# Performance work log

Hardware: AMD Instinct MI355X
Metric: run time of the kernel (lower is better)

The kernel has to match this reference:

```python
import jax, jax.numpy as jnp
import numpy as np

D = 2048        # input_size / model dim
H = 2816        # hidden_size per expert (GLU -> w1 has 2*H rows)
E = 8           # num_experts
M = 4096        # tokens (batch*seq)


def setup_inputs() -> dict:
    key = jax.random.key(0)
    k1, k2, k3, k4, k5 = jax.random.split(key, 5)
    x = jax.random.normal(k1, (M, D), dtype=jnp.float32)
    # ParallelExperts init: uniform(-1/fan_in_dim, 1/fan_in_dim); scale kept simple here
    w1 = jax.random.uniform(k2, (E, 2 * H, D), dtype=jnp.float32, minval=-1.0, maxval=1.0) / (2 * H)
    w2 = jax.random.uniform(k3, (E, D, H), dtype=jnp.float32, minval=-1.0, maxval=1.0) / D
    router_w = jax.random.normal(k4, (E, D), dtype=jnp.float32) * (1.0 / np.sqrt(D))
    bias = jnp.zeros((D,), dtype=jnp.float32)
    return {"x": x, "w1": w1, "w2": w2, "router_w": router_w, "bias": bias, "top_k": 2}


def _moe_forward(x, w1, w2, router_w, bias, top_k):
    # Router: logits -> softmax (fp32) -> top-k -> renormalize (fused_moe semantics)
    logits = x @ router_w.T                                # [M, E]
    probs = jax.nn.softmax(logits.astype(jnp.float32), axis=-1)
    topk_w, topk_ids = jax.lax.top_k(probs, top_k)         # [M, k]
    topk_w = topk_w / jnp.sum(topk_w, axis=-1, keepdims=True)
    # Dense combine weights [M, E]: gate weight if expert selected, else 0
    m = x.shape[0]
    combine = jnp.zeros((m, w1.shape[0]), dtype=x.dtype)
    combine = combine.at[jnp.arange(m)[:, None], topk_ids].add(topk_w.astype(x.dtype))
    # Grouped expert GEMMs, expressed as a loop over the small fixed expert set.
    # Contribution of expert e is masked by combine[:, e] (zero for unrouted tokens).
    y = jnp.zeros_like(x)
    hdim = w2.shape[2]
    for e in range(w1.shape[0]):
        g = x @ w1[e].T                                    # [M, 2H]
        h = jax.nn.silu(g[:, :hdim]) * g[:, hdim:]          # silu_and_mul (GLU)
        y = y + combine[:, e:e + 1] * (h @ w2[e].T)         # [M, D]
    return y + bias


def reference(x, w1, w2, router_w, bias, top_k):
    return _moe_forward(x, w1, w2, router_w, bias, top_k)
```

## Files before the change

### kernel.cpp

```cpp
#include <hip/hip_runtime.h>
#include <hip/hip_bf16.h>
#include <stdint.h>

#define M_TOK 4096
#define DDIM  2048
#define HDIM  2816
#define NEXP  8
#define PMAX  10240
#define MAXTILES 40
#define NB1   22
#define NB2   8
#define NT1   64
#define NT2   88

typedef __attribute__((ext_vector_type(8))) short short8;
typedef __attribute__((ext_vector_type(4))) float f32x4;

#define GLD16(g, l) __builtin_amdgcn_global_load_lds(                              \
    (const __attribute__((address_space(1))) unsigned int*)(g),                    \
    (__attribute__((address_space(3))) unsigned int*)(l), 16, 0, 0)

#define VMCNT(n) asm volatile("s_waitcnt vmcnt(" #n ")" ::: "memory")

__device__ __forceinline__ unsigned short f2bf(float f) {
  unsigned int u = __float_as_uint(f);
  u += 0x7fffu + ((u >> 16) & 1u);
  return (unsigned short)(u >> 16);
}
__device__ __forceinline__ float bf2f(unsigned short u) {
  return __uint_as_float(((unsigned)u) << 16);
}

#define GP0(KT, VM, STG)                                                         \
  { VMCNT(VM);                                                                   \
    __builtin_amdgcn_s_barrier();                                                \
    asm volatile("" ::: "memory");                                               \
    { const char* ab_ = ldsp + ((KT) & 3) * 16384;                               \
      const char* bb_ = ldsp + 65536 + ((KT) & 3) * 16384;                       \
      _Pragma("unroll") for (int mi = 0; mi < 4; ++mi)                           \
        av[mi] = *(const short8*)(ab_ + aoff[mi]);                               \
      _Pragma("unroll") for (int ni = 0; ni < 4; ++ni)                           \
        bv[ni] = *(const short8*)(bb_ + boff[ni]);                               \
      if (STG) { size_t kb_ = (size_t)((KT) + 3) * 64;                           \
        char* d_ = ldsp + (((KT) + 3) & 3) * 16384;                              \
        GLD16(aS0 + kb_, d_ + aD0); GLD16(aS1 + kb_, d_ + aD1); }                \
    }                                                                            \
    asm volatile("" ::: "memory");                                               \
    __builtin_amdgcn_s_barrier();                                                \
    __builtin_amdgcn_s_setprio(1);                                               \
    _Pragma("unroll") for (int mi = 0; mi < 4; ++mi)                             \
      _Pragma("unroll") for (int ni = 0; ni < 4; ++ni)                           \
        acc[mi][ni] = __builtin_amdgcn_mfma_f32_16x16x32_bf16(av[mi], bv[ni], acc[mi][ni], 0, 0, 0); \
    __builtin_amdgcn_s_setprio(0); }

#define GP1(KT, STG)                                                             \
  { __builtin_amdgcn_s_barrier();                                                \
    asm volatile("" ::: "memory");                                               \
    { const char* ab_ = ldsp + ((KT) & 3) * 16384;                               \
      _Pragma("unroll") for (int mi = 0; mi < 4; ++mi)                           \
        av[mi] = *(const short8*)(ab_ + aoff[4 + mi]);                           \
      if (STG) { size_t kb_ = (size_t)((KT) + 3) * 64;                           \
        char* d_ = ldsp + 65536 + (((KT) + 3) & 3) * 16384;                      \
        GLD16(bS0 + kb_, d_ + aD0); GLD16(bS1 + kb_, d_ + aD1); }                \
    }                                                                            \
    asm volatile("" ::: "memory");                                               \
    __builtin_amdgcn_s_barrier();                                                \
    __builtin_amdgcn_s_setprio(1);                                               \
    _Pragma("unroll") for (int mi = 0; mi < 4; ++mi)                             \
      _Pragma("unroll") for (int ni = 0; ni < 4; ++ni)                           \
        acc[4 + mi][ni] = __builtin_amdgcn_mfma_f32_16x16x32_bf16(av[mi], bv[ni], acc[4 + mi][ni], 0, 0, 0); \
    __builtin_amdgcn_s_setprio(0); }

__global__ void cvt_bf16_k(const float4* __restrict__ in, ushort4* __restrict__ out, int n4) {
  int stride = gridDim.x * blockDim.x;
  for (int i = blockIdx.x * blockDim.x + threadIdx.x; i < n4; i += stride) {
    float4 v = in[i];
    ushort4 o;
    o.x = f2bf(v.x); o.y = f2bf(v.y); o.z = f2bf(v.z); o.w = f2bf(v.w);
    out[i] = o;
  }
}

__global__ void init_k(int* __restrict__ tok, int* __restrict__ counts, int* __restrict__ cursors) {
  int i = blockIdx.x * blockDim.x + threadIdx.x;
  if (i < PMAX) tok[i] = -1;
  if (i < NEXP) { counts[i] = 0; cursors[i] = 0; }
}

__global__ __launch_bounds__(256) void router_k(const float4* __restrict__ x4,
                                                const float4* __restrict__ rw4,
                                                ushort4* __restrict__ xb4,
                                                float* __restrict__ wgt,
                                                int* __restrict__ eid,
                                                int* __restrict__ counts) {
  int lane = threadIdx.x & 63;
  int wv = threadIdx.x >> 6;
  int t = blockIdx.x * 4 + wv;
  int base = t * (DDIM / 4);
  float acc[NEXP];
#pragma unroll
  for (int e = 0; e < NEXP; ++e) acc[e] = 0.f;
#pragma unroll
  for (int j = 0; j < DDIM / 4 / 64; ++j) {
    float4 v = x4[base + j * 64 + lane];
    ushort4 o;
    o.x = f2bf(v.x); o.y = f2bf(v.y); o.z = f2bf(v.z); o.w = f2bf(v.w);
    xb4[base + j * 64 + lane] = o;
#pragma unroll
    for (int e = 0; e < NEXP; ++e) {
      float4 w = rw4[e * (DDIM / 4) + j * 64 + lane];
      acc[e] += v.x * w.x + v.y * w.y + v.z * w.z + v.w * w.w;
    }
  }
#pragma unroll
  for (int e = 0; e < NEXP; ++e) {
#pragma unroll
    for (int s = 32; s > 0; s >>= 1) acc[e] += __shfl_xor(acc[e], s, 64);
  }
  if (lane == 0) {
    float mx = acc[0];
#pragma unroll
    for (int e = 1; e < NEXP; ++e) mx = fmaxf(mx, acc[e]);
    float p[NEXP];
#pragma unroll
    for (int e = 0; e < NEXP; ++e) p[e] = expf(acc[e] - mx);
    int e0 = 0; float p0 = p[0];
#pragma unroll
    for (int e = 1; e < NEXP; ++e) if (p[e] > p0) { p0 = p[e]; e0 = e; }
    int e1 = -1; float p1 = -1.f;
#pragma unroll
    for (int e = 0; e < NEXP; ++e) if (e != e0 && p[e] > p1) { p1 = p[e]; e1 = e; }
    float s = p0 + p1;
    wgt[2 * t] = p0 / s; wgt[2 * t + 1] = p1 / s;
    eid[2 * t] = e0;     eid[2 * t + 1] = e1;
    atomicAdd(&counts[e0], 1);
    atomicAdd(&counts[e1], 1);
  }
}

__global__ void offsets_k(const int* __restrict__ counts, int* __restrict__ offs,
                          int* __restrict__ tile2exp, int* __restrict__ tilerow,
                          int* __restrict__ ntiles) {
  if (threadIdx.x == 0 && blockIdx.x == 0) {
    int o = 0, nt = 0;
    for (int e = 0; e < NEXP; ++e) {
      offs[e] = o;
      int c = counts[e];
      int pt = (c + 255) >> 8;
      for (int i = 0; i < pt; ++i) { tile2exp[nt] = e; tilerow[nt] = o + i * 256; ++nt; }
      o += pt << 8;
    }
    offs[NEXP] = o;
    ntiles[0] = nt;
  }
}

__global__ void scatter_k(const int* __restrict__ eid, const int* __restrict__ offs,
                          int* __restrict__ cursors, int* __restrict__ tok,
                          int* __restrict__ slot) {
  int t = blockIdx.x * blockDim.x + threadIdx.x;
  if (t >= M_TOK) return;
#pragma unroll
  for (int k = 0; k < 2; ++k) {
    int e = eid[2 * t + k];
    int p = offs[e] + atomicAdd(&cursors[e], 1);
    tok[p] = t;
    slot[2 * t + k] = p;
  }
}

__global__ __launch_bounds__(512, 1) void gemm1_k(const unsigned short* __restrict__ xb,
                                                  const unsigned short* __restrict__ w1b,
                                                  const int* __restrict__ tok,
                                                  const int* __restrict__ tile2exp,
                                                  const int* __restrict__ tilerow,
                                                  const int* __restrict__ ntiles,
                                                  unsigned short* __restrict__ h) {
  __shared__ char ldsp[131072];
  int mt = blockIdx.x;
  if (mt >= ntiles[0]) return;
  int e = tile2exp[mt], r0 = tilerow[mt];
  int n0 = blockIdx.y * 128;
  int tid = threadIdx.x, lane = tid & 63;
  int wv = tid >> 6, wm = wv >> 2, wn = wv & 3;
  int l15 = lane & 15, g = lane >> 4;

  int row0 = tid >> 2, g0 = (tid & 3) ^ ((row0 >> 1) & 3);
  int row1 = row0 + 128;
  int t0 = tok[r0 + row0]; if (t0 < 0) t0 = 0;
  int t1 = tok[r0 + row1]; if (t1 < 0) t1 = 0;
  const char* aS0 = (const char*)xb + (size_t)t0 * (DDIM * 2) + g0 * 16;
  const char* aS1 = (const char*)xb + (size_t)t1 * (DDIM * 2) + g0 * 16;
  size_t w1r0 = (size_t)e * (2 * HDIM) +
                (row0 < 128 ? (size_t)(n0 + row0) : (size_t)(HDIM + n0 + row0 - 128));
  size_t w1r1 = (size_t)e * (2 * HDIM) + (size_t)(HDIM + n0 + row1 - 128);
  const char* bS0 = (const char*)w1b + w1r0 * (DDIM * 2) + g0 * 16;
  const char* bS1 = (const char*)w1b + w1r1 * (DDIM * 2) + g0 * 16;
  int aD0 = tid * 16, aD1 = 8192 + tid * 16;

  int aoff[8], boff[4];
#pragma unroll
  for (int mi = 0; mi < 8; ++mi) {
    int r = wm * 128 + mi * 16 + l15;
    aoff[mi] = r * 64 + ((g ^ ((r >> 1) & 3)) * 16);
  }
#pragma unroll
  for (int ni = 0; ni < 4; ++ni) {
    int r = wn * 64 + ni * 16 + l15;
    boff[ni] = r * 64 + ((g ^ ((r >> 1) & 3)) * 16);
  }

  f32x4 acc[8][4];
#pragma unroll
  for (int mi = 0; mi < 8; ++mi)
#pragma unroll
    for (int ni = 0; ni < 4; ++ni) acc[mi][ni] = (f32x4)(0.f);

  short8 av[4], bv[4];

#pragma unroll
  for (int t = 0; t < 3; ++t) {
    GLD16(aS0 + (size_t)t * 64, ldsp + t * 16384 + aD0);
    GLD16(aS1 + (size_t)t * 64, ldsp + t * 16384 + aD1);
    GLD16(bS0 + (size_t)t * 64, ldsp + 65536 + t * 16384 + aD0);
    GLD16(bS1 + (size_t)t * 64, ldsp + 65536 + t * 16384 + aD1);
  }

  for (int kt = 0; kt < NT1 - 3; ++kt) { GP0(kt, 8, 1); GP1(kt, 1); }
  GP0(NT1 - 3, 8, 0); GP1(NT1 - 3, 0);
  GP0(NT1 - 2, 4, 0); GP1(NT1 - 2, 0);
  GP0(NT1 - 1, 0, 0); GP1(NT1 - 1, 0);

  __syncthreads();
  float* xch = (float*)ldsp;
  int rbase = (lane >> 4) * 4;
  if (wn >= 2) {
    int uc0 = (wn - 2) * 64;
#pragma unroll
    for (int mi = 0; mi < 8; ++mi)
#pragma unroll
      for (int ni = 0; ni < 4; ++ni)
#pragma unroll
        for (int j = 0; j < 4; ++j) {
          int r = wm * 128 + mi * 16 + rbase + j;
          int c = uc0 + ni * 16 + l15;
          int cs = c ^ ((r & 3) << 2) ^ ((r & 1) << 4);
          xch[r * 128 + cs] = acc[mi][ni][j];
        }
  }
  __syncthreads();
  if (wn < 2) {
#pragma unroll
    for (int mi = 0; mi < 8; ++mi)
#pragma unroll
      for (int ni = 0; ni < 4; ++ni)
#pragma unroll
        for (int j = 0; j < 4; ++j) {
          int r = wm * 128 + mi * 16 + rbase + j;
          int c = wn * 64 + ni * 16 + l15;
          int cs = c ^ ((r & 3) << 2) ^ ((r & 1) << 4);
          float gg = acc[mi][ni][j];
          float u = xch[r * 128 + cs];
          float sv = gg / (1.f + expf(-gg));
          h[(size_t)(r0 + r) * HDIM + n0 + c] = f2bf(sv * u);
        }
  }
}

__global__ __launch_bounds__(512, 1) void gemm2_k(const unsigned short* __restrict__ h,
                                                  const unsigned short* __restrict__ w2b,
                                                  const int* __restrict__ tile2exp,
                                                  const int* __restrict__ tilerow,
                                                  const int* __restrict__ ntiles,
                                                  unsigned short* __restrict__ yp) {
  __shared__ char ldsp[131072];
  int mt = blockIdx.x;
  if (mt >= ntiles[0]) return;
  int e = tile2exp[mt], r0 = tilerow[mt];
  int n0 = blockIdx.y * 256;
  int tid = threadIdx.x, lane = tid & 63;
  int wv = tid >> 6, wm = wv >> 2, wn = wv & 3;
  int l15 = lane & 15, g = lane >> 4;

  int row0 = tid >> 2, g0 = (tid & 3) ^ ((row0 >> 1) & 3);
  int row1 = row0 + 128;
  const char* aS0 = (const char*)h + (size_t)(r0 + row0) * (HDIM * 2) + g0 * 16;
  const char* aS1 = (const char*)h + (size_t)(r0 + row1) * (HDIM * 2) + g0 * 16;
  const char* bS0 = (const char*)w2b + ((size_t)e * DDIM + n0 + row0) * (HDIM * 2) + g0 * 16;
  const char* bS1 = (const char*)w2b + ((size_t)e * DDIM + n0 + row1) * (HDIM * 2) + g0 * 16;
  int aD0 = tid * 16, aD1 = 8192 + tid * 16;

  int aoff[8], boff[4];
#pragma unroll
  for (int mi = 0; mi < 8; ++mi) {
    int r = wm * 128 + mi * 16 + l15;
    aoff[mi] = r * 64 + ((g ^ ((r >> 1) & 3)) * 16);
  }
#pragma unroll
  for (int ni = 0; ni < 4; ++ni) {
    int r = wn * 64 + ni * 16 + l15;
    boff[ni] = r * 64 + ((g ^ ((r >> 1) & 3)) * 16);
  }

  f32x4 acc[8][4];
#pragma unroll
  for (int mi = 0; mi < 8; ++mi)
#pragma unroll
    for (int ni = 0; ni < 4; ++ni) acc[mi][ni] = (f32x4)(0.f);

  short8 av[4], bv[4];

#pragma unroll
  for (int t = 0; t < 3; ++t) {
    GLD16(aS0 + (size_t)t * 64, ldsp + t * 16384 + aD0);
    GLD16(aS1 + (size_t)t * 64, ldsp + t * 16384 + aD1);
    GLD16(bS0 + (size_t)t * 64, ldsp + 65536 + t * 16384 + aD0);
    GLD16(bS1 + (size_t)t * 64, ldsp + 65536 + t * 16384 + aD1);
  }

  for (int kt = 0; kt < NT2 - 3; ++kt) { GP0(kt, 8, 1); GP1(kt, 1); }
  GP0(NT2 - 3, 8, 0); GP1(NT2 - 3, 0);
  GP0(NT2 - 2, 4, 0); GP1(NT2 - 2, 0);
  GP0(NT2 - 1, 0, 0); GP1(NT2 - 1, 0);

  int rbase = (lane >> 4) * 4;
#pragma unroll
  for (int mi = 0; mi < 8; ++mi)
#pragma unroll
    for (int ni = 0; ni < 4; ++ni)
#pragma unroll
      for (int j = 0; j < 4; ++j) {
        int r = r0 + wm * 128 + mi * 16 + rbase + j;
        int c = n0 + wn * 64 + ni * 16 + l15;
        yp[(size_t)r * DDIM + c] = f2bf(acc[mi][ni][j]);
      }
}

__global__ void combine_k(const unsigned short* __restrict__ yp, const float* __restrict__ wgt,
                          const int* __restrict__ slot, const float* __restrict__ bias,
                          float* __restrict__ out) {
  int idx = blockIdx.x * blockDim.x + threadIdx.x;
  int t = idx >> 8, q = (idx & 255) * 8;
  float w0 = wgt[2 * t], w1 = wgt[2 * t + 1];
  int s0 = slot[2 * t], s1 = slot[2 * t + 1];
  short8 a8 = *(const short8*)(yp + (size_t)s0 * DDIM + q);
  short8 b8 = *(const short8*)(yp + (size_t)s1 * DDIM + q);
  float* op = out + (size_t)t * DDIM + q;
#pragma unroll
  for (int k = 0; k < 8; ++k) {
    float av = bf2f((unsigned short)a8[k]);
    float bv = bf2f((unsigned short)b8[k]);
    op[k] = w0 * av + w1 * bv + bias[q + k];
  }
}

extern "C" void kernel_launch(void* const* d_in, const int* in_sizes, int n_in,
                              void* d_out, int out_size, void* d_ws, size_t ws_size,
                              hipStream_t stream) {
  const float* x    = (const float*)d_in[0];
  const float* w1   = (const float*)d_in[1];
  const float* w2   = (const float*)d_in[2];
  const float* rw   = (const float*)d_in[3];
  const float* bias = (const float*)d_in[4];
  float* out = (float*)d_out;

  char* ws = (char*)d_ws;
  size_t off = 0;
  auto alloc = [&](size_t bytes) -> void* {
    void* p = ws + off;
    off = (off + bytes + 255) & ~(size_t)255;
    return p;
  };
  unsigned short* w1b = (unsigned short*)alloc((size_t)NEXP * 2 * HDIM * DDIM * 2);
  unsigned short* w2b = (unsigned short*)alloc((size_t)NEXP * DDIM * HDIM * 2);
  unsigned short* xb  = (unsigned short*)alloc((size_t)M_TOK * DDIM * 2);
  unsigned short* h   = (unsigned short*)alloc((size_t)PMAX * HDIM * 2);
  unsigned short* yp  = (unsigned short*)alloc((size_t)PMAX * DDIM * 2);
  float* wgt          = (float*)alloc((size_t)M_TOK * 2 * 4);
  int* eid            = (int*)alloc((size_t)M_TOK * 2 * 4);
  int* slot           = (int*)alloc((size_t)M_TOK * 2 * 4);
  int* tok            = (int*)alloc((size_t)PMAX * 4);
  int* counts         = (int*)alloc(64 * 4);
  int* cursors        = (int*)alloc(64 * 4);
  int* offs           = (int*)alloc(64 * 4);
  int* ntiles         = (int*)alloc(64 * 4);
  int* tile2exp       = (int*)alloc(128 * 4);
  int* tilerow        = (int*)alloc(128 * 4);

  hipLaunchKernelGGL(init_k, dim3((PMAX + 255) / 256), dim3(256), 0, stream, tok, counts, cursors);
  hipLaunchKernelGGL(cvt_bf16_k, dim3(2048), dim3(256), 0, stream,
                     (const float4*)w1, (ushort4*)w1b, (int)((size_t)NEXP * 2 * HDIM * DDIM / 4));
  hipLaunchKernelGGL(cvt_bf16_k, dim3(2048), dim3(256), 0, stream,
                     (const float4*)w2, (ushort4*)w2b, (int)((size_t)NEXP * DDIM * HDIM / 4));
  hipLaunchKernelGGL(router_k, dim3(M_TOK / 4), dim3(256), 0, stream,
                     (const float4*)x, (const float4*)rw, (ushort4*)xb, wgt, eid, counts);
  hipLaunchKernelGGL(offsets_k, dim3(1), dim3(64), 0, stream, counts, offs,
                     tile2exp, tilerow, ntiles);
  hipLaunchKernelGGL(scatter_k, dim3((M_TOK + 255) / 256), dim3(256), 0, stream, eid, offs, cursors, tok, slot);
  hipLaunchKernelGGL(gemm1_k, dim3(MAXTILES, NB1), dim3(512), 0, stream,
                     xb, w1b, tok, tile2exp, tilerow, ntiles, h);
  hipLaunchKernelGGL(gemm2_k, dim3(MAXTILES, NB2), dim3(512), 0, stream,
                     h, w2b, tile2exp, tilerow, ntiles, yp);
  hipLaunchKernelGGL(combine_k, dim3(M_TOK * (DDIM / 8) / 256), dim3(256), 0, stream, yp, wgt, slot, bias, out);
}
```

Measured before the change: 757.2 us.

## Restructure GEMM main loops into K=128 ping-pong tiles with interleaved staging

Replaces the four-stage K=64 ring-buffer pipeline in both expert GEMM kernels with a two-buffer ping-pong scheme over K=128 tiles. Each tile is split into four sub-phases that interleave LDS reads, async global-to-LDS loads for the next tile, and 16-MFMA bursts separated by barriers. The w1 row mapping for the gate/up halves is simplified to match the new staging. The aim is to cut the number of vmcnt waits per K step and overlap loads better with MFMA, at the cost of more barriers and a tighter dependency schedule that is easy to get wrong.

```diff
diff --git a/kernel.cpp b/kernel.cpp
--- a/kernel.cpp
+++ b/kernel.cpp
@@ -10,8 +10,8 @@
 #define MAXTILES 40
 #define NB1   22
 #define NB2   8
-#define NT1   64
-#define NT2   88
+#define NKT1  32
+#define NKT2  44
 
 typedef __attribute__((ext_vector_type(8))) short short8;
 typedef __attribute__((ext_vector_type(4))) float f32x4;
@@ -31,45 +31,54 @@
   return __uint_as_float(((unsigned)u) << 16);
 }
 
-#define GP0(KT, VM, STG)                                                         \
-  { VMCNT(VM);                                                                   \
-    __builtin_amdgcn_s_barrier();                                                \
-    asm volatile("" ::: "memory");                                               \
-    { const char* ab_ = ldsp + ((KT) & 3) * 16384;                               \
-      const char* bb_ = ldsp + 65536 + ((KT) & 3) * 16384;                       \
-      _Pragma("unroll") for (int mi = 0; mi < 4; ++mi)                           \
-        av[mi] = *(const short8*)(ab_ + aoff[mi]);                               \
-      _Pragma("unroll") for (int ni = 0; ni < 4; ++ni)                           \
-        bv[ni] = *(const short8*)(bb_ + boff[ni]);                               \
-      if (STG) { size_t kb_ = (size_t)((KT) + 3) * 64;                           \
-        char* d_ = ldsp + (((KT) + 3) & 3) * 16384;                              \
-        GLD16(aS0 + kb_, d_ + aD0); GLD16(aS1 + kb_, d_ + aD1); }                \
-    }                                                                            \
-    asm volatile("" ::: "memory");                                               \
-    __builtin_amdgcn_s_barrier();                                                \
-    __builtin_amdgcn_s_setprio(1);                                               \
-    _Pragma("unroll") for (int mi = 0; mi < 4; ++mi)                             \
-      _Pragma("unroll") for (int ni = 0; ni < 4; ++ni)                           \
-        acc[mi][ni] = __builtin_amdgcn_mfma_f32_16x16x32_bf16(av[mi], bv[ni], acc[mi][ni], 0, 0, 0); \
+
+#define STGA(TT, PP, S)                                                            \
+  { size_t kb_ = (size_t)(TT) * 128 + (S) * 64;                                    \
+    char* d_ = ldsp + (PP) * 32768 + (S) * 16384;                                  \
+    GLD16(aS0 + kb_, d_ + tid * 16); GLD16(aS1 + kb_, d_ + 8192 + tid * 16); }
+
+#define STGB(TT, PP, S)                                                            \
+  { size_t kb_ = (size_t)(TT) * 128 + (S) * 64;                                    \
+    char* d_ = ldsp + 65536 + (PP) * 32768 + (S) * 16384;                          \
+    GLD16(bS0 + kb_, d_ + tid * 16); GLD16(bS1 + kb_, d_ + 8192 + tid * 16); }
+
+#define DSRA(PP, S, M)                                                             \
+  { const char* ab_ = ldsp + (PP) * 32768 + (S) * 16384;                           \
+    _Pragma("unroll") for (int j_ = 0; j_ < 4; ++j_)                               \
+      av[j_] = *(const short8*)(ab_ + aoff[(M) * 4 + j_]); }
+
+#define DSRB(PP, S)                                                                \
+  { const char* bb_ = ldsp + 65536 + (PP) * 32768 + (S) * 16384;                   \
+    _Pragma("unroll") for (int j_ = 0; j_ < 4; ++j_)                               \
+      bv[j_] = *(const short8*)(bb_ + boff[j_]); }
+
+#define MMA16(M)                                                                   \
+  { __builtin_amdgcn_s_setprio(1);                                                 \
+    _Pragma("unroll") for (int j_ = 0; j_ < 4; ++j_)                               \
+      _Pragma("unroll") for (int n_ = 0; n_ < 4; ++n_)                             \
+        acc[(M) * 4 + j_][n_] =                                                    \
+          __builtin_amdgcn_mfma_f32_16x16x32_bf16(av[j_], bv[n_], acc[(M)*4+j_][n_], 0, 0, 0); \
     __builtin_amdgcn_s_setprio(0); }
 
-#define GP1(KT, STG)                                                             \
-  { __builtin_amdgcn_s_barrier();                                                \
-    asm volatile("" ::: "memory");                                               \
-    { const char* ab_ = ldsp + ((KT) & 3) * 16384;                               \
-      _Pragma("unroll") for (int mi = 0; mi < 4; ++mi)                           \
-        av[mi] = *(const short8*)(ab_ + aoff[4 + mi]);                           \
-      if (STG) { size_t kb_ = (size_t)((KT) + 3) * 64;                           \
-        char* d_ = ldsp + 65536 + (((KT) + 3) & 3) * 16384;                      \
-        GLD16(bS0 + kb_, d_ + aD0); GLD16(bS1 + kb_, d_ + aD1); }                \
-    }                                                                            \
-    asm volatile("" ::: "memory");                                               \
-    __builtin_amdgcn_s_barrier();                                                \
-    __builtin_amdgcn_s_setprio(1);                                               \
-    _Pragma("unroll") for (int mi = 0; mi < 4; ++mi)                             \
-      _Pragma("unroll") for (int ni = 0; ni < 4; ++ni)                           \
-        acc[4 + mi][ni] = __builtin_amdgcn_mfma_f32_16x16x32_bf16(av[mi], bv[ni], acc[4 + mi][ni], 0, 0, 0); \
-    __builtin_amdgcn_s_setprio(0); }
+#define KTILE(T, P, S0, S1, S2, S3, VM)                                            \
+  {                       \
+    DSRA(P, 0, 0); DSRB(P, 0);                                                     \
+    if (S0) STGA((T) + 1, (P) ^ 1, 1);                                             \
+    __builtin_amdgcn_s_barrier(); MMA16(0); __builtin_amdgcn_s_barrier();          \
+                          \
+    DSRA(P, 0, 1);                                                                 \
+    if (S1) STGB((T) + 2, P, 0);                                                   \
+    __builtin_amdgcn_s_barrier(); MMA16(1); __builtin_amdgcn_s_barrier();          \
+                          \
+    DSRA(P, 1, 0); DSRB(P, 1);                                                     \
+    if (S2) STGA((T) + 2, P, 0);                                                   \
+    __builtin_amdgcn_s_barrier(); MMA16(0); __builtin_amdgcn_s_barrier();          \
+        \
+    DSRA(P, 1, 1);                                                                 \
+    if (S3) STGB((T) + 2, P, 1);                                                   \
+    __builtin_amdgcn_s_barrier(); MMA16(1);                                        \
+    VMCNT(VM);                                                                     \
+    __builtin_amdgcn_s_barrier(); }
 
 __global__ void cvt_bf16_k(const float4* __restrict__ in, ushort4* __restrict__ out, int n4) {
   int stride = gridDim.x * blockDim.x;
@@ -191,23 +200,21 @@
   int t1 = tok[r0 + row1]; if (t1 < 0) t1 = 0;
   const char* aS0 = (const char*)xb + (size_t)t0 * (DDIM * 2) + g0 * 16;
   const char* aS1 = (const char*)xb + (size_t)t1 * (DDIM * 2) + g0 * 16;
-  size_t w1r0 = (size_t)e * (2 * HDIM) +
-                (row0 < 128 ? (size_t)(n0 + row0) : (size_t)(HDIM + n0 + row0 - 128));
-  size_t w1r1 = (size_t)e * (2 * HDIM) + (size_t)(HDIM + n0 + row1 - 128);
+  size_t w1r0 = (size_t)e * (2 * HDIM) + (size_t)(n0 + row0);
+  size_t w1r1 = (size_t)e * (2 * HDIM) + (size_t)(HDIM + n0 + row0);
   const char* bS0 = (const char*)w1b + w1r0 * (DDIM * 2) + g0 * 16;
   const char* bS1 = (const char*)w1b + w1r1 * (DDIM * 2) + g0 * 16;
-  int aD0 = tid * 16, aD1 = 8192 + tid * 16;
 
   int aoff[8], boff[4];
 #pragma unroll
   for (int mi = 0; mi < 8; ++mi) {
     int r = wm * 128 + mi * 16 + l15;
-    aoff[mi] = r * 64 + ((g ^ ((r >> 1) & 3)) * 16);
+    aoff[mi] = r * 64 + ((g ^ ((r >> 1) & 3)) << 4);
   }
 #pragma unroll
   for (int ni = 0; ni < 4; ++ni) {
     int r = wn * 64 + ni * 16 + l15;
-    boff[ni] = r * 64 + ((g ^ ((r >> 1) & 3)) * 16);
+    boff[ni] = r * 64 + ((g ^ ((r >> 1) & 3)) << 4);
   }
 
   f32x4 acc[8][4];
@@ -218,18 +225,18 @@
 
   short8 av[4], bv[4];
 
-#pragma unroll
-  for (int t = 0; t < 3; ++t) {
-    GLD16(aS0 + (size_t)t * 64, ldsp + t * 16384 + aD0);
-    GLD16(aS1 + (size_t)t * 64, ldsp + t * 16384 + aD1);
-    GLD16(bS0 + (size_t)t * 64, ldsp + 65536 + t * 16384 + aD0);
-    GLD16(bS1 + (size_t)t * 64, ldsp + 65536 + t * 16384 + aD1);
-  }
-
-  for (int kt = 0; kt < NT1 - 3; ++kt) { GP0(kt, 8, 1); GP1(kt, 1); }
-  GP0(NT1 - 3, 8, 0); GP1(NT1 - 3, 0);
-  GP0(NT1 - 2, 4, 0); GP1(NT1 - 2, 0);
-  GP0(NT1 - 1, 0, 0); GP1(NT1 - 1, 0);
+  STGA(0, 0, 0); STGB(0, 0, 0); STGA(0, 0, 1); STGB(0, 0, 1);
+  STGB(1, 1, 0); STGA(1, 1, 0); STGB(1, 1, 1);
+  VMCNT(6);
+  __builtin_amdgcn_s_barrier();
+
+#pragma unroll 1
+  for (int t = 0; t < NKT1 - 2; t += 2) {
+    KTILE(t, 0, 1, 1, 1, 1, 6);
+    KTILE(t + 1, 1, 1, 1, 1, 1, 6);
+  }
+  KTILE(NKT1 - 2, 0, 1, 0, 0, 0, 0);
+  KTILE(NKT1 - 1, 1, 0, 0, 0, 0, 0);
 
   __syncthreads();
   float* xch = (float*)ldsp;
@@ -288,18 +295,17 @@
   const char* aS1 = (const char*)h + (size_t)(r0 + row1) * (HDIM * 2) + g0 * 16;
   const char* bS0 = (const char*)w2b + ((size_t)e * DDIM + n0 + row0) * (HDIM * 2) + g0 * 16;
   const char* bS1 = (const char*)w2b + ((size_t)e * DDIM + n0 + row1) * (HDIM * 2) + g0 * 16;
-  int aD0 = tid * 16, aD1 = 8192 + tid * 16;
 
   int aoff[8], boff[4];
 #pragma unroll
   for (int mi = 0; mi < 8; ++mi) {
     int r = wm * 128 + mi * 16 + l15;
-    aoff[mi] = r * 64 + ((g ^ ((r >> 1) & 3)) * 16);
+    aoff[mi] = r * 64 + ((g ^ ((r >> 1) & 3)) << 4);
   }
 #pragma unroll
   for (int ni = 0; ni < 4; ++ni) {
     int r = wn * 64 + ni * 16 + l15;
-    boff[ni] = r * 64 + ((g ^ ((r >> 1) & 3)) * 16);
+    boff[ni] = r * 64 + ((g ^ ((r >> 1) & 3)) << 4);
   }
 
   f32x4 acc[8][4];
@@ -310,18 +316,18 @@
 
   short8 av[4], bv[4];
 
-#pragma unroll
-  for (int t = 0; t < 3; ++t) {
-    GLD16(aS0 + (size_t)t * 64, ldsp + t * 16384 + aD0);
-    GLD16(aS1 + (size_t)t * 64, ldsp + t * 16384 + aD1);
-    GLD16(bS0 + (size_t)t * 64, ldsp + 65536 + t * 16384 + aD0);
-    GLD16(bS1 + (size_t)t * 64, ldsp + 65536 + t * 16384 + aD1);
-  }
-
-  for (int kt = 0; kt < NT2 - 3; ++kt) { GP0(kt, 8, 1); GP1(kt, 1); }
-  GP0(NT2 - 3, 8, 0); GP1(NT2 - 3, 0);
-  GP0(NT2 - 2, 4, 0); GP1(NT2 - 2, 0);
-  GP0(NT2 - 1, 0, 0); GP1(NT2 - 1, 0);
+  STGA(0, 0, 0); STGB(0, 0, 0); STGA(0, 0, 1); STGB(0, 0, 1);
+  STGB(1, 1, 0); STGA(1, 1, 0); STGB(1, 1, 1);
+  VMCNT(6);
+  __builtin_amdgcn_s_barrier();
+
+#pragma unroll 1
+  for (int t = 0; t < NKT2 - 2; t += 2) {
+    KTILE(t, 0, 1, 1, 1, 1, 6);
+    KTILE(t + 1, 1, 1, 1, 1, 1, 6);
+  }
+  KTILE(NKT2 - 2, 0, 1, 0, 0, 0, 0);
+  KTILE(NKT2 - 1, 1, 0, 0, 0, 0, 0);
 
   int rbase = (lane >> 4) * 4;
 #pragma unroll
```

After: 750.6 us. Within noise of the previous version (-0.9%).
